# Kernel optimization log

Measured on AMD Instinct MI355X. Metric: run time of the kernel, lower is better.

Reference implementation:

```python
import jax, jax.numpy as jnp
import numpy as np

NUM_EMB = 1000
HIDDEN = 256
SCALE = 2
N_HEADS = 8
HEAD_DIM = HIDDEN * SCALE // N_HEADS  # 64
HS = HIDDEN * SCALE  # 512
EPS = 1e-6


def setup_inputs() -> dict:
    key = jax.random.key(0)
    ks = jax.random.split(key, 12)
    B, N, C, H, W = 8, 8, HIDDEN, 32, 32
    std = 0.02
    return {
        "q": jax.random.randint(ks[0], (B,), 0, NUM_EMB, dtype=jnp.int32),
        "c": jax.random.normal(ks[1], (B, N, C, H, W), dtype=jnp.float32),
        "rms_w": jnp.ones((HIDDEN,), dtype=jnp.float32),
        "emb": jax.random.normal(ks[2], (NUM_EMB, HIDDEN), dtype=jnp.float32) * std,
        "w1": jax.random.normal(ks[3], (HIDDEN, HS), dtype=jnp.float32) * std,
        "b1": jnp.zeros((HS,), dtype=jnp.float32),
        "w2": jax.random.normal(ks[4], (HS, HS), dtype=jnp.float32) * std,
        "b2": jnp.zeros((HS,), dtype=jnp.float32),
        "w_kv": jax.random.normal(ks[5], (HIDDEN, HS * 2), dtype=jnp.float32) * std,
        "w_out": jax.random.normal(ks[6], (HS, HIDDEN), dtype=jnp.float32) * std,
        "b_out": jnp.zeros((HIDDEN,), dtype=jnp.float32),
    }


def reference(q, c, rms_w, emb, w1, b1, w2, b2, w_kv, w_out, b_out):
    B, N, C, H, W = c.shape
    attn_scale = HEAD_DIM ** (-0.5)
    # permute to [B,H,W,N,C] and RMSNorm over channel dim
    c = jnp.transpose(c, (0, 3, 4, 1, 2))
    c = c * jax.lax.rsqrt(jnp.mean(c * c, axis=-1, keepdims=True) + EPS) * rms_w
    # query path: embed + gated MLP -> [B, n_heads, head_dim]
    qe = emb[q]                                   # [B, hidden]
    qh = jax.nn.silu(qe @ w1 + b1) @ w2 + b2      # [B, HS]
    qh = qh.reshape(B, N_HEADS, HEAD_DIM)
    # kv projection: [B,H,W,N, 2*HS] -> [B,H,W,n_heads,N, 2*head_dim]
    kv = (c @ w_kv).reshape(B, H, W, N, N_HEADS, 2 * HEAD_DIM)
    kv = jnp.transpose(kv, (0, 1, 2, 4, 3, 5))
    k, v = jnp.split(kv, 2, axis=-1)              # each [B,H,W,heads,N,head_dim]
    # broadcast per-pixel cross-attention: query shared over H,W
    dots = jnp.einsum('bed,bhwend->bhwen', qh, k) * attn_scale
    attn = jax.nn.softmax(dots, axis=-1)
    h = jnp.einsum('bhwen,bhwend->bhwed', attn, v)  # [B,H,W,heads,head_dim]
    h = h.reshape(B, H, W, HS)
    out = h @ w_out + b_out                        # [B,H,W,hidden]
    return jnp.transpose(out, (0, 3, 1, 2))        # [B,hidden,H,W]
```

## Files before the change

### kernel.cpp

```cpp
#include <hip/hip_runtime.h>

typedef _Float16 f16;
typedef _Float16 f16x4 __attribute__((ext_vector_type(4)));
typedef _Float16 f16x8 __attribute__((ext_vector_type(8)));
typedef float f32x4 __attribute__((ext_vector_type(4)));

#define NR 264
#define AP 2120

__launch_bounds__(256)
__global__ void k_setup1(const int* __restrict__ q, const float* __restrict__ emb,
                         const float* __restrict__ w1, const float* __restrict__ b1,
                         const float* __restrict__ w_kv, const float* __restrict__ w_out,
                         const float* __restrict__ rms_w,
                         float* __restrict__ x1ws, f16* __restrict__ mt) {
    int blk = blockIdx.x;
    int t = threadIdx.x;
    __shared__ float qe[256];
    __shared__ float ps[8][32];
    __shared__ float wv[64][8];

    if (blk < 128) {
        int b = blk >> 4, ot = blk & 15;
        qe[t] = emb[(size_t)q[b] * 256 + t];
        __syncthreads();
        int o = ot * 32 + (t & 31), ks = t >> 5;
        float acc = 0.f;
        for (int c = ks * 32; c < ks * 32 + 32; ++c)
            acc += qe[c] * w1[c * 512 + o];
        ps[ks][t & 31] = acc;
        __syncthreads();
        if (t < 32) {
            float v = b1[ot * 32 + t];
#pragma unroll
            for (int k = 0; k < 8; ++k) v += ps[k][t];
            x1ws[b * 512 + ot * 32 + t] = v / (1.f + __expf(-v));
        }
    } else {
        int mb = blk - 128;
        int e = mb >> 5, c0 = (mb & 31) * 8;
        {
            int d = t & 63, cc = t >> 6;
            wv[d][cc]     = w_kv[(size_t)(c0 + cc) * 1024 + e * 128 + 64 + d];
            wv[d][cc + 4] = w_kv[(size_t)(c0 + cc + 4) * 1024 + e * 128 + 64 + d];
        }
        __syncthreads();
        int o = t;
        float acc[8];
#pragma unroll
        for (int c = 0; c < 8; ++c) acc[c] = 0.f;
        for (int d = 0; d < 64; ++d) {
            float wo = w_out[(size_t)(e * 64 + d) * 256 + o];
            float4 wa = *(const float4*)&wv[d][0];
            float4 wb = *(const float4*)&wv[d][4];
            acc[0] += wa.x * wo; acc[1] += wa.y * wo; acc[2] += wa.z * wo; acc[3] += wa.w * wo;
            acc[4] += wb.x * wo; acc[5] += wb.y * wo; acc[6] += wb.z * wo; acc[7] += wb.w * wo;
        }
        f16x8 ov;
#pragma unroll
        for (int c = 0; c < 8; ++c) ov[c] = (f16)(acc[c] * rms_w[c0 + c]);
        *(f16x8*)(mt + (size_t)o * 2048 + e * 256 + c0) = ov;
    }
}

__launch_bounds__(256)
__global__ void k_qkh(const float* __restrict__ x1ws, const float* __restrict__ w2,
                      const float* __restrict__ b2, const float* __restrict__ w_kv,
                      const float* __restrict__ rms_w, f16* __restrict__ qkw) {
    int b = blockIdx.x >> 3, e = blockIdx.x & 7;
    int t = threadIdx.x;
    __shared__ float x1L[512];
    __shared__ float ps[4][64];
    __shared__ float qhL[64];
    x1L[t]       = x1ws[b * 512 + t];
    x1L[t + 256] = x1ws[b * 512 + t + 256];
    __syncthreads();
    int d = t & 63, ks = t >> 6;
    float acc = 0.f;
    for (int k = ks * 128; k < ks * 128 + 128; ++k)
        acc += x1L[k] * w2[k * 512 + e * 64 + d];
    ps[ks][d] = acc;
    __syncthreads();
    if (t < 64)
        qhL[t] = b2[e * 64 + t] + ps[0][t] + ps[1][t] + ps[2][t] + ps[3][t];
    __syncthreads();
    const float* row = w_kv + (size_t)t * 1024 + e * 128;
    float a2 = 0.f;
#pragma unroll
    for (int dd = 0; dd < 64; dd += 4) {
        float4 wv4 = *(const float4*)(row + dd);
        a2 += qhL[dd] * wv4.x + qhL[dd + 1] * wv4.y + qhL[dd + 2] * wv4.z + qhL[dd + 3] * wv4.w;
    }
    qkw[(b * 8 + e) * 256 + t] = (f16)(a2 * rms_w[t]);
}

__launch_bounds__(512, 4)
__global__ void k_attn(const float* __restrict__ cin, const f16* __restrict__ qkw,
                       const f16* __restrict__ mt, const float* __restrict__ b_out,
                       float* __restrict__ out) {
    int blk = blockIdx.x;
    int b = blk & 7;
    int hw0 = (blk >> 3) * 16;
    int t = threadIdx.x;
    int lane = t & 63, w = t >> 6;
    int m16 = lane & 15, quad = lane >> 4;

    __shared__ f16 A[16 * AP];
    __shared__ float dotsP[16][8][8];
    __shared__ float wred[8][8][4][4];
    __shared__ float rinvL[16][8];

    const float* cb = cin + ((size_t)b * 8 * 256) * 1024 + hw0;
    for (int g = 0; g < 8; ++g) {
        f32x4 s = {0.f, 0.f, 0.f, 0.f};
#pragma unroll
        for (int i = 0; i < 2; ++i) {
            int idx = t + i * 512;
            int ch = idx >> 2, pxg = idx & 3;
            float4 v = *(const float4*)(cb + ((size_t)(g * 256 + ch) << 10) + pxg * 4);
            int base = g * NR + ch;
            A[(pxg * 4 + 0) * AP + base] = (f16)v.x;
            A[(pxg * 4 + 1) * AP + base] = (f16)v.y;
            A[(pxg * 4 + 2) * AP + base] = (f16)v.z;
            A[(pxg * 4 + 3) * AP + base] = (f16)v.w;
            s[0] += v.x * v.x; s[1] += v.y * v.y; s[2] += v.z * v.z; s[3] += v.w * v.w;
        }
#pragma unroll
        for (int m = 4; m <= 32; m <<= 1) {
            s[0] += __shfl_xor(s[0], m); s[1] += __shfl_xor(s[1], m);
            s[2] += __shfl_xor(s[2], m); s[3] += __shfl_xor(s[3], m);
        }
        if (lane < 4) *(f32x4*)&wred[w][g][lane][0] = s;
    }
    __syncthreads();

    if (t < 128) {
        int p = t >> 3, n = t & 7;
        float ss = 0.f;
#pragma unroll
        for (int ww = 0; ww < 8; ++ww) ss += wred[ww][n][p >> 2][p & 3];
        rinvL[p][n] = rsqrtf(ss * (1.f / 256.f) + 1e-6f);
    }
    {
        f32x4 d0 = {0.f, 0.f, 0.f, 0.f};
        const f16* qrow = qkw + (size_t)b * 2048 + (m16 & 7) * 256;
        const f16* arow = &A[m16 * AP + w * NR];
#pragma unroll
        for (int ks = 0; ks < 8; ++ks) {
            f16x8 a0  = *(const f16x8*)(arow + ks * 32 + quad * 8);
            f16x8 bfr = *(const f16x8*)(qrow + ks * 32 + quad * 8);
            d0 = __builtin_amdgcn_mfma_f32_16x16x32_f16(a0, bfr, d0, 0, 0, 0);
        }
        if (m16 < 8) {
#pragma unroll
            for (int r = 0; r < 4; ++r) dotsP[quad * 4 + r][w][m16] = d0[r];
        }
    }
    __syncthreads();

    if (t < 128) {
        int p = t >> 3, e = t & 7;
        float l[8];
#pragma unroll
        for (int n = 0; n < 8; ++n) l[n] = dotsP[p][n][e] * rinvL[p][n] * 0.125f;
        float mx = l[0];
#pragma unroll
        for (int n = 1; n < 8; ++n) mx = fmaxf(mx, l[n]);
        float s = 0.f;
#pragma unroll
        for (int n = 0; n < 8; ++n) { l[n] = __expf(l[n] - mx); s += l[n]; }
        float inv = 1.f / s;
#pragma unroll
        for (int n = 0; n < 8; ++n) dotsP[p][n][e] = l[n] * inv * rinvL[p][n];
    }
    __syncthreads();

    {
        int px = t & 15, c0 = (t >> 4) * 8;
        float at[8][8];
#pragma unroll
        for (int e = 0; e < 8; ++e)
#pragma unroll
            for (int n = 0; n < 8; ++n) at[e][n] = dotsP[px][n][e];
#pragma unroll
        for (int cc = 0; cc < 8; cc += 4) {
            int c = c0 + cc;
            float cv[8][4];
#pragma unroll
            for (int n = 0; n < 8; ++n) {
                f16x4 hv = *(const f16x4*)&A[px * AP + n * NR + c];
                cv[n][0] = (float)hv[0]; cv[n][1] = (float)hv[1];
                cv[n][2] = (float)hv[2]; cv[n][3] = (float)hv[3];
            }
#pragma unroll
            for (int e = 0; e < 8; ++e) {
                float r0 = 0.f, r1 = 0.f, r2 = 0.f, r3 = 0.f;
#pragma unroll
                for (int n = 0; n < 8; ++n) {
                    float an = at[e][n];
                    r0 += an * cv[n][0]; r1 += an * cv[n][1];
                    r2 += an * cv[n][2]; r3 += an * cv[n][3];
                }
                f16x4 ov; ov[0] = (f16)r0; ov[1] = (f16)r1; ov[2] = (f16)r2; ov[3] = (f16)r3;
                *(f16x4*)&A[px * AP + e * NR + c] = ov;
            }
        }
    }
    __syncthreads();

    {
        f32x4 acc[2];
        acc[0] = (f32x4){0.f, 0.f, 0.f, 0.f};
        acc[1] = (f32x4){0.f, 0.f, 0.f, 0.f};
#pragma unroll 8
        for (int ks = 0; ks < 64; ++ks) {
            f16x8 af = *(const f16x8*)&A[m16 * AP + (ks >> 3) * NR + (ks & 7) * 32 + quad * 8];
#pragma unroll
            for (int ot = 0; ot < 2; ++ot) {
                f16x8 bfr = *(const f16x8*)(mt + (size_t)(w * 32 + ot * 16 + m16) * 2048
                                            + ks * 32 + quad * 8);
                acc[ot] = __builtin_amdgcn_mfma_f32_16x16x32_f16(af, bfr, acc[ot], 0, 0, 0);
            }
        }
#pragma unroll
        for (int ot = 0; ot < 2; ++ot) {
            int o = w * 32 + ot * 16 + m16;
            float bo = b_out[o];
            float4 vv = {acc[ot][0] + bo, acc[ot][1] + bo, acc[ot][2] + bo, acc[ot][3] + bo};
            *(float4*)(out + ((size_t)b * 256 + o) * 1024 + hw0 + quad * 4) = vv;
        }
    }
}

extern "C" void kernel_launch(void* const* d_in, const int* in_sizes, int n_in,
                              void* d_out, int out_size, void* d_ws, size_t ws_size,
                              hipStream_t stream) {
    (void)in_sizes; (void)n_in; (void)out_size; (void)ws_size;
    const int*   q     = (const int*)d_in[0];
    const float* c     = (const float*)d_in[1];
    const float* rms_w = (const float*)d_in[2];
    const float* emb   = (const float*)d_in[3];
    const float* w1    = (const float*)d_in[4];
    const float* b1    = (const float*)d_in[5];
    const float* w2    = (const float*)d_in[6];
    const float* b2    = (const float*)d_in[7];
    const float* w_kv  = (const float*)d_in[8];
    const float* w_out = (const float*)d_in[9];
    const float* b_out = (const float*)d_in[10];
    float* out = (float*)d_out;

    char* ws = (char*)d_ws;
    float* x1ws = (float*)ws;
    f16*   qkw  = (f16*)(ws + 16384);
    f16*   mt   = (f16*)(ws + 49152);

    k_setup1<<<384, 256, 0, stream>>>(q, emb, w1, b1, w_kv, w_out, rms_w, x1ws, mt);
    k_qkh   <<<64, 256, 0, stream>>>(x1ws, w2, b2, w_kv, rms_w, qkw);
    k_attn  <<<512, 512, 0, stream>>>(c, qkw, mt, b_out, out);
}
```

Measured before the change: 201.3 us.

## Fuse query MLP kernels into setup and swizzle attention LDS layout

Merges the two small query-path kernels into one setup kernel, so each (batch, head) block recomputes the full first MLP layer itself instead of going through a workspace round trip and an extra launch. Separately, the attention kernel's shared-memory tile switches from a padded row layout to an XOR-swizzled 4KB-per-pixel layout, meant to avoid LDS bank conflicts on the MFMA fragment loads. The trade-off is that the first MLP layer is now computed redundantly, eight times per batch, and fewer blocks run it serially over 256 inputs.

```diff
diff --git a/kernel.cpp b/kernel.cpp
--- a/kernel.cpp
+++ b/kernel.cpp
@@ -5,39 +5,57 @@
 typedef _Float16 f16x8 __attribute__((ext_vector_type(8)));
 typedef float f32x4 __attribute__((ext_vector_type(4)));
 
-#define NR 264
-#define AP 2120
+static __device__ inline char* a_addr(char* Abase, int px, int k) {
+    return Abase + px * 4096 + ((((k >> 3) ^ (px & 7)) << 4) | ((k & 7) << 1));
+}
 
 __launch_bounds__(256)
-__global__ void k_setup1(const int* __restrict__ q, const float* __restrict__ emb,
-                         const float* __restrict__ w1, const float* __restrict__ b1,
-                         const float* __restrict__ w_kv, const float* __restrict__ w_out,
-                         const float* __restrict__ rms_w,
-                         float* __restrict__ x1ws, f16* __restrict__ mt) {
+__global__ void k_setup(const int* __restrict__ q, const float* __restrict__ emb,
+                        const float* __restrict__ w1, const float* __restrict__ b1,
+                        const float* __restrict__ w2, const float* __restrict__ b2,
+                        const float* __restrict__ w_kv, const float* __restrict__ w_out,
+                        const float* __restrict__ rms_w,
+                        f16* __restrict__ qkw, f16* __restrict__ mt) {
     int blk = blockIdx.x;
     int t = threadIdx.x;
     __shared__ float qe[256];
-    __shared__ float ps[8][32];
+    __shared__ float x1L[512];
+    __shared__ float ps[4][64];
+    __shared__ float qhL[64];
     __shared__ float wv[64][8];
 
-    if (blk < 128) {
-        int b = blk >> 4, ot = blk & 15;
+    if (blk < 64) {
+        int b = blk >> 3, e = blk & 7;
         qe[t] = emb[(size_t)q[b] * 256 + t];
         __syncthreads();
-        int o = ot * 32 + (t & 31), ks = t >> 5;
+        float a0 = b1[t], a1 = b1[t + 256];
+        for (int c = 0; c < 256; ++c) {
+            float qv = qe[c];
+            a0 += qv * w1[c * 512 + t];
+            a1 += qv * w1[c * 512 + t + 256];
+        }
+        x1L[t]       = a0 / (1.f + __expf(-a0));
+        x1L[t + 256] = a1 / (1.f + __expf(-a1));
+        __syncthreads();
+        int d = t & 63, ks = t >> 6;
         float acc = 0.f;
-        for (int c = ks * 32; c < ks * 32 + 32; ++c)
-            acc += qe[c] * w1[c * 512 + o];
-        ps[ks][t & 31] = acc;
-        __syncthreads();
-        if (t < 32) {
-            float v = b1[ot * 32 + t];
-#pragma unroll
-            for (int k = 0; k < 8; ++k) v += ps[k][t];
-            x1ws[b * 512 + ot * 32 + t] = v / (1.f + __expf(-v));
-        }
+        for (int k = ks * 128; k < ks * 128 + 128; ++k)
+            acc += x1L[k] * w2[k * 512 + e * 64 + d];
+        ps[ks][d] = acc;
+        __syncthreads();
+        if (t < 64)
+            qhL[t] = b2[e * 64 + t] + ps[0][t] + ps[1][t] + ps[2][t] + ps[3][t];
+        __syncthreads();
+        const float* row = w_kv + (size_t)t * 1024 + e * 128;
+        float a2 = 0.f;
+#pragma unroll
+        for (int dd = 0; dd < 64; dd += 4) {
+            float4 wv4 = *(const float4*)(row + dd);
+            a2 += qhL[dd] * wv4.x + qhL[dd + 1] * wv4.y + qhL[dd + 2] * wv4.z + qhL[dd + 3] * wv4.w;
+        }
+        qkw[(b * 8 + e) * 256 + t] = (f16)(a2 * rms_w[t]);
     } else {
-        int mb = blk - 128;
+        int mb = blk - 64;
         int e = mb >> 5, c0 = (mb & 31) * 8;
         {
             int d = t & 63, cc = t >> 6;
@@ -61,37 +79,6 @@
         for (int c = 0; c < 8; ++c) ov[c] = (f16)(acc[c] * rms_w[c0 + c]);
         *(f16x8*)(mt + (size_t)o * 2048 + e * 256 + c0) = ov;
     }
-}
-
-__launch_bounds__(256)
-__global__ void k_qkh(const float* __restrict__ x1ws, const float* __restrict__ w2,
-                      const float* __restrict__ b2, const float* __restrict__ w_kv,
-                      const float* __restrict__ rms_w, f16* __restrict__ qkw) {
-    int b = blockIdx.x >> 3, e = blockIdx.x & 7;
-    int t = threadIdx.x;
-    __shared__ float x1L[512];
-    __shared__ float ps[4][64];
-    __shared__ float qhL[64];
-    x1L[t]       = x1ws[b * 512 + t];
-    x1L[t + 256] = x1ws[b * 512 + t + 256];
-    __syncthreads();
-    int d = t & 63, ks = t >> 6;
-    float acc = 0.f;
-    for (int k = ks * 128; k < ks * 128 + 128; ++k)
-        acc += x1L[k] * w2[k * 512 + e * 64 + d];
-    ps[ks][d] = acc;
-    __syncthreads();
-    if (t < 64)
-        qhL[t] = b2[e * 64 + t] + ps[0][t] + ps[1][t] + ps[2][t] + ps[3][t];
-    __syncthreads();
-    const float* row = w_kv + (size_t)t * 1024 + e * 128;
-    float a2 = 0.f;
-#pragma unroll
-    for (int dd = 0; dd < 64; dd += 4) {
-        float4 wv4 = *(const float4*)(row + dd);
-        a2 += qhL[dd] * wv4.x + qhL[dd + 1] * wv4.y + qhL[dd + 2] * wv4.z + qhL[dd + 3] * wv4.w;
-    }
-    qkw[(b * 8 + e) * 256 + t] = (f16)(a2 * rms_w[t]);
 }
 
 __launch_bounds__(512, 4)
@@ -105,7 +92,7 @@
     int lane = t & 63, w = t >> 6;
     int m16 = lane & 15, quad = lane >> 4;
 
-    __shared__ f16 A[16 * AP];
+    __shared__ char A[16 * 4096];
     __shared__ float dotsP[16][8][8];
     __shared__ float wred[8][8][4][4];
     __shared__ float rinvL[16][8];
@@ -118,11 +105,11 @@
             int idx = t + i * 512;
             int ch = idx >> 2, pxg = idx & 3;
             float4 v = *(const float4*)(cb + ((size_t)(g * 256 + ch) << 10) + pxg * 4);
-            int base = g * NR + ch;
-            A[(pxg * 4 + 0) * AP + base] = (f16)v.x;
-            A[(pxg * 4 + 1) * AP + base] = (f16)v.y;
-            A[(pxg * 4 + 2) * AP + base] = (f16)v.z;
-            A[(pxg * 4 + 3) * AP + base] = (f16)v.w;
+            int k = g * 256 + ch;
+            *(f16*)a_addr(A, pxg * 4 + 0, k) = (f16)v.x;
+            *(f16*)a_addr(A, pxg * 4 + 1, k) = (f16)v.y;
+            *(f16*)a_addr(A, pxg * 4 + 2, k) = (f16)v.z;
+            *(f16*)a_addr(A, pxg * 4 + 3, k) = (f16)v.w;
             s[0] += v.x * v.x; s[1] += v.y * v.y; s[2] += v.z * v.z; s[3] += v.w * v.w;
         }
 #pragma unroll
@@ -144,10 +131,9 @@
     {
         f32x4 d0 = {0.f, 0.f, 0.f, 0.f};
         const f16* qrow = qkw + (size_t)b * 2048 + (m16 & 7) * 256;
-        const f16* arow = &A[m16 * AP + w * NR];
 #pragma unroll
         for (int ks = 0; ks < 8; ++ks) {
-            f16x8 a0  = *(const f16x8*)(arow + ks * 32 + quad * 8);
+            f16x8 a0  = *(const f16x8*)a_addr(A, m16, w * 256 + ks * 32 + quad * 8);
             f16x8 bfr = *(const f16x8*)(qrow + ks * 32 + quad * 8);
             d0 = __builtin_amdgcn_mfma_f32_16x16x32_f16(a0, bfr, d0, 0, 0, 0);
         }
@@ -188,7 +174,7 @@
             float cv[8][4];
 #pragma unroll
             for (int n = 0; n < 8; ++n) {
-                f16x4 hv = *(const f16x4*)&A[px * AP + n * NR + c];
+                f16x4 hv = *(const f16x4*)a_addr(A, px, n * 256 + c);
                 cv[n][0] = (float)hv[0]; cv[n][1] = (float)hv[1];
                 cv[n][2] = (float)hv[2]; cv[n][3] = (float)hv[3];
             }
@@ -202,7 +188,7 @@
                     r2 += an * cv[n][2]; r3 += an * cv[n][3];
                 }
                 f16x4 ov; ov[0] = (f16)r0; ov[1] = (f16)r1; ov[2] = (f16)r2; ov[3] = (f16)r3;
-                *(f16x4*)&A[px * AP + e * NR + c] = ov;
+                *(f16x4*)a_addr(A, px, e * 256 + c) = ov;
             }
         }
     }
@@ -214,7 +200,8 @@
         acc[1] = (f32x4){0.f, 0.f, 0.f, 0.f};
 #pragma unroll 8
         for (int ks = 0; ks < 64; ++ks) {
-            f16x8 af = *(const f16x8*)&A[m16 * AP + (ks >> 3) * NR + (ks & 7) * 32 + quad * 8];
+            int k = (ks >> 3) * 256 + (ks & 7) * 32 + quad * 8;
+            f16x8 af = *(const f16x8*)a_addr(A, m16, k);
 #pragma unroll
             for (int ot = 0; ot < 2; ++ot) {
                 f16x8 bfr = *(const f16x8*)(mt + (size_t)(w * 32 + ot * 16 + m16) * 2048
@@ -250,11 +237,9 @@
     float* out = (float*)d_out;
 
     char* ws = (char*)d_ws;
-    float* x1ws = (float*)ws;
-    f16*   qkw  = (f16*)(ws + 16384);
-    f16*   mt   = (f16*)(ws + 49152);
-
-    k_setup1<<<384, 256, 0, stream>>>(q, emb, w1, b1, w_kv, w_out, rms_w, x1ws, mt);
-    k_qkh   <<<64, 256, 0, stream>>>(x1ws, w2, b2, w_kv, rms_w, qkw);
-    k_attn  <<<512, 512, 0, stream>>>(c, qkw, mt, b_out, out);
-}
+    f16* qkw = (f16*)ws;
+    f16* mt  = (f16*)(ws + 32768);
+
+    k_setup<<<320, 256, 0, stream>>>(q, emb, w1, b1, w2, b2, w_kv, w_out, rms_w, qkw, mt);
+    k_attn <<<512, 512, 0, stream>>>(c, qkw, mt, b_out, out);
+}
```

Result: slower. 210.0 us (+4.3%).
